# Kernel optimization log

Hardware: AMD Instinct MI355X
Metric: run time of the kernel (lower is better)

The kernel has to match this reference:

```python
import jax, jax.numpy as jnp
import numpy as np

TPB = 64          # tokens_per_block
SUB = 16          # sub_chunk_size
BUDGET = 1024     # dynamic_sparse_token_budget
ROPE_BASE = 10000.0
NEG = -1e9


def rope_neox(x, pos, base=ROPE_BASE):
    # neox-style rotary over full head_dim, single position `pos`
    D = x.shape[-1]
    half = D // 2
    inv_freq = 1.0 / (base ** (jnp.arange(half, dtype=jnp.float32) * (2.0 / D)))
    ang = pos * inv_freq
    c, s = jnp.cos(ang), jnp.sin(ang)
    x1, x2 = x[..., :half], x[..., half:]
    return jnp.concatenate([x1 * c - x2 * s, x1 * s + x2 * c], axis=-1)


def setup_inputs() -> dict:
    key = jax.random.key(0)
    ks = jax.random.split(key, 8)
    B, H, Hkv, D = 4, 32, 8, 128
    P, S = 128, 64  # pages, tokens per page (memory_max_len=8192)
    q = jax.random.normal(ks[0], (B, H, D), dtype=jnp.float32)
    k = jax.random.normal(ks[1], (B, Hkv, D), dtype=jnp.float32)
    v = jax.random.normal(ks[2], (B, Hkv, D), dtype=jnp.float32)
    k_cache = jax.random.randint(ks[3], (B, P, S, Hkv, D), 0, 127, dtype=jnp.int32)
    v_cache = jax.random.randint(ks[4], (B, P, S, Hkv, D), 0, 127, dtype=jnp.int32)
    # per-tensor dequant scales for K and V (realistic small magnitudes)
    kv_scale_quant_orig = jax.random.uniform(ks[5], (2,), dtype=jnp.float32) * 0.02 + 0.005
    lengths_per_sample = jax.random.randint(ks[6], (4,), 4096, 8192, dtype=jnp.int32)
    return {
        'q': q, 'k': k, 'v': v,
        'kv_scale_quant_orig': kv_scale_quant_orig,
        'k_cache': k_cache, 'v_cache': v_cache,
        'lengths_per_sample': lengths_per_sample,
        'timestep': 8192,
    }


def reference(q, k, v, kv_scale_quant_orig, k_cache, v_cache, lengths_per_sample, timestep):
    B, H, D = q.shape
    Hkv = k.shape[1]
    G = H // Hkv  # GQA group size
    P, S = k_cache.shape[1], k_cache.shape[2]
    sm_scale = 1.0 / np.sqrt(D)
    pos = float(timestep - 1)  # rope_scaling_factor = 1.0

    # rotary on current query and current key
    qh = rope_neox(q, pos).reshape(B, Hkv, G, D)
    k_cur = rope_neox(k, pos)

    # int8 per-tensor dequant of paged KV cache -> [B, Hkv, P, S, D]
    sk, sv = kv_scale_quant_orig[0], kv_scale_quant_orig[1]
    kc = k_cache.astype(jnp.float32).transpose(0, 3, 1, 2, 4) * sk
    vc = v_cache.astype(jnp.float32).transpose(0, 3, 1, 2, 4) * sv

    lengths = jnp.maximum(lengths_per_sample, 1)

    # ---- dynamic top-k page selection (selector pass over full cache) ----
    scores = jnp.einsum('bhgd,bhpsd->bhgps', qh, kc) * sm_scale  # [B,Hkv,G,P,S]
    posgrid = jnp.arange(P * S, dtype=jnp.int32).reshape(P, S)
    valid = posgrid[None, None, None] < lengths[:, None, None, None, None]
    scores = jnp.where(valid, scores, NEG)
    # sub-chunk max stats then per-page max (== max over all tokens in page)
    page_stats = scores.reshape(B, Hkv, G, P, S // SUB, SUB).max(axis=-1).max(axis=-1)  # [B,Hkv,G,P]
    kk = min(max(3, BUDGET // TPB), P) - 1
    _, top_idx = jax.lax.top_k(page_stats[..., :-1], kk)
    last = jnp.full(top_idx.shape[:-1] + (1,), P - 1, dtype=top_idx.dtype)
    sel = jnp.concatenate([top_idx, last], axis=-1)  # [B,Hkv,G,Kp], last page forced
    Kp = sel.shape[-1]

    # ---- sparse attention over the selected pages + current token ----
    idx = sel[..., None, None]  # [B,Hkv,G,Kp,1,1]
    k_sel = jnp.take_along_axis(kc[:, :, None], idx, axis=3)  # [B,Hkv,G,Kp,S,D]
    v_sel = jnp.take_along_axis(vc[:, :, None], idx, axis=3)

    sel_scores = jnp.einsum('bhgd,bhgksd->bhgks', qh, k_sel) * sm_scale
    sel_pos = sel[..., None] * TPB + jnp.arange(S, dtype=jnp.int32)
    smask = sel_pos < lengths[:, None, None, None, None]
    sel_scores = jnp.where(smask, sel_scores, NEG)

    cur_score = jnp.einsum('bhgd,bhd->bhg', qh, k_cur) * sm_scale
    all_scores = jnp.concatenate(
        [sel_scores.reshape(B, Hkv, G, Kp * S), cur_score[..., None]], axis=-1)
    p = jax.nn.softmax(all_scores, axis=-1)

    v_all = jnp.concatenate(
        [v_sel.reshape(B, Hkv, G, Kp * S, D),
         jnp.broadcast_to(v[:, :, None, None, :], (B, Hkv, G, 1, D))], axis=3)
    out = jnp.einsum('bhgt,bhgtd->bhgd', p, v_all).reshape(B, H, D)
    selected_page_idx = sel.reshape(B, H, Kp).astype(jnp.int32)
    return out, selected_page_idx
```

## Files before the change

### kernel.cpp

```cpp
#include <hip/hip_runtime.h>
#include <hip/hip_bf16.h>

#define NB 4
#define NH 32
#define NHKV 8
#define NG 4
#define ND 128
#define NP 128
#define NS 64
#define KK 15
#define KP 16
#define NEGF -1000000000.0f
#define SM_SCALE 0.088388347648318447f

#define WS_QH   0
#define WS_KR   16384
#define WS_CUR  20480
#define WS_SC   20992
#define WS_ST   (WS_SC + NB*NHKV*NG*NP*NS)
#define WS_SEL  (WS_ST + NB*NHKV*NG*NP)
#define WS_PW   (WS_SEL + NB*NHKV*NG*KP)

__global__ __launch_bounds__(256) void prep_kernel(const float* __restrict__ q,
                                                   const float* __restrict__ k,
                                                   const int* __restrict__ tstep,
                                                   float* __restrict__ ws) {
    float* QH = ws + WS_QH;
    float* KR = ws + WS_KR;
    float* CUR = ws + WS_CUR;
    const float pos = (float)(tstep[0] - 1);
    const int tid = threadIdx.x;
    for (int i = tid; i < NB * NH * 64; i += 256) {
        int j = i & 63, head = i >> 6;
        float invf = 1.0f / powf(10000.0f, (float)j * (1.0f / 64.0f));
        float sng, csn;
        sincosf(pos * invf, &sng, &csn);
        float x1 = q[head * ND + j], x2 = q[head * ND + 64 + j];
        QH[head * ND + j] = x1 * csn - x2 * sng;
        QH[head * ND + 64 + j] = x1 * sng + x2 * csn;
    }
    for (int i = tid; i < NB * NHKV * 64; i += 256) {
        int j = i & 63, head = i >> 6;
        float invf = 1.0f / powf(10000.0f, (float)j * (1.0f / 64.0f));
        float sng, csn;
        sincosf(pos * invf, &sng, &csn);
        float x1 = k[head * ND + j], x2 = k[head * ND + 64 + j];
        KR[head * ND + j] = x1 * csn - x2 * sng;
        KR[head * ND + 64 + j] = x1 * sng + x2 * csn;
    }
    __syncthreads();
    for (int h = tid; h < NB * NH; h += 256) {
        int b = h >> 5, hh = h & 31, hkv = hh >> 2;
        const float* qr = QH + h * ND;
        const float* kr = KR + (b * NHKV + hkv) * ND;
        float acc = 0.f;
#pragma unroll 8
        for (int d = 0; d < ND; ++d) acc += qr[d] * kr[d];
        CUR[h] = acc * SM_SCALE;
    }
}

__global__ __launch_bounds__(256) void score_kernel(const int* __restrict__ kc,
                                                    const float* __restrict__ kvs,
                                                    const int* __restrict__ lens,
                                                    float* __restrict__ ws) {
    __shared__ float klds[NS][132];
    __shared__ float qlds[NG][ND];
    const float* QH = ws + WS_QH;
    float* SC = ws + WS_SC;
    float* ST = ws + WS_ST;
    const int blk = blockIdx.x;
    const int p = blk & (NP - 1);
    const int bh = blk >> 7;
    const int hkv = bh & (NHKV - 1);
    const int b = bh >> 3;
    const int len = max(lens[b], 1);
    const int tid = threadIdx.x;
    const int g = tid >> 6, s = tid & 63;
    const int bhg = (b * NHKV + hkv) * NG + g;
    if (p * NS >= len) {
        SC[bhg * (NP * NS) + p * NS + s] = NEGF;
        if (s == 0) ST[bhg * NP + p] = NEGF;
        return;
    }
    for (int i = tid; i < NG * ND; i += 256)
        qlds[i >> 7][i & 127] = QH[(b * NH + hkv * NG + (i >> 7)) * ND + (i & 127)];
    const int4* src = (const int4*)(kc + ((b * NP + p) * NS * NHKV + hkv) * ND);
    for (int i = tid; i < NS * 32; i += 256) {
        int ss = i >> 5, j = i & 31;
        int4 w = src[ss * (NHKV * ND / 4) + j];
        float4 f;
        f.x = (float)w.x; f.y = (float)w.y; f.z = (float)w.z; f.w = (float)w.w;
        *(float4*)&klds[ss][j * 4] = f;
    }
    __syncthreads();
    const float4* qrow = (const float4*)qlds[g];
    const float4* krow = (const float4*)&klds[s][0];
    float acc = 0.f;
#pragma unroll
    for (int j = 0; j < 32; ++j) {
        float4 qa = qrow[j], ka = krow[j];
        acc += qa.x * ka.x + qa.y * ka.y + qa.z * ka.z + qa.w * ka.w;
    }
    float score = acc * kvs[0] * SM_SCALE;
    if (p * NS + s >= len) score = NEGF;
    SC[bhg * (NP * NS) + p * NS + s] = score;
    float m = score;
#pragma unroll
    for (int off = 32; off; off >>= 1) m = fmaxf(m, __shfl_xor(m, off));
    if (s == 0) ST[bhg * NP + p] = m;
}

__global__ __launch_bounds__(256) void select_kernel(const float* __restrict__ v,
                                                     const float* __restrict__ kvs,
                                                     float* __restrict__ ws,
                                                     float* __restrict__ out) {
    const int bhg = blockIdx.x;
    const int b = bhg >> 5;
    const int hkv = (bhg >> 2) & 7;
    const int tid = threadIdx.x;
    const float* SC = ws + WS_SC;
    const float* ST = ws + WS_ST;
    const float* CUR = ws + WS_CUR;
    int* SEL = (int*)(ws + WS_SEL);
    float* PW = ws + WS_PW;
    __shared__ float st[NP];
    __shared__ int sel[KP];
    __shared__ float redm[4], reds[4];
    if (tid < NP) st[tid] = (tid < NP - 1) ? ST[bhg * NP + tid] : NEGF;
    __syncthreads();
    if (tid < 64) {
        for (int r = 0; r < KK; ++r) {
            float v1 = st[tid];
            int i1 = tid;
            float v2 = st[tid + 64];
            int i2 = tid + 64;
            if (v2 > v1) { v1 = v2; i1 = i2; }
#pragma unroll
            for (int off = 32; off; off >>= 1) {
                float ov = __shfl_xor(v1, off);
                int oi = __shfl_xor(i1, off);
                if (ov > v1 || (ov == v1 && oi < i1)) { v1 = ov; i1 = oi; }
            }
            if (tid == 0) sel[r] = i1;
            st[i1] = NEGF;
        }
        if (tid == 0) sel[KK] = NP - 1;
    }
    __syncthreads();
    if (tid < KP) {
        out[NB * NH * ND + bhg * KP + tid] = (float)sel[tid];
        SEL[bhg * KP + tid] = sel[tid];
    }
    float vals[4];
    float lm = NEGF;
    const float* scb = SC + bhg * (NP * NS);
#pragma unroll
    for (int u = 0; u < 4; ++u) {
        int idx = tid * 4 + u;
        int j = idx >> 6, s2 = idx & 63;
        float sc = scb[sel[j] * NS + s2];
        vals[u] = sc;
        lm = fmaxf(lm, sc);
    }
#pragma unroll
    for (int off = 32; off; off >>= 1) lm = fmaxf(lm, __shfl_xor(lm, off));
    if ((tid & 63) == 0) redm[tid >> 6] = lm;
    __syncthreads();
    const float cur = CUR[bhg];
    float m = fmaxf(fmaxf(redm[0], redm[1]), fmaxf(redm[2], redm[3]));
    m = fmaxf(m, cur);
    float e[4];
    float ls = 0.f;
#pragma unroll
    for (int u = 0; u < 4; ++u) {
        e[u] = expf(vals[u] - m);
        ls += e[u];
    }
#pragma unroll
    for (int off = 32; off; off >>= 1) ls += __shfl_xor(ls, off);
    if ((tid & 63) == 0) reds[tid >> 6] = ls;
    __syncthreads();
    float ecur = expf(cur - m);
    float Z = reds[0] + reds[1] + reds[2] + reds[3] + ecur;
    float inv = 1.0f / Z;
    float pscale = inv * kvs[1];
#pragma unroll
    for (int u = 0; u < 4; ++u) PW[bhg * 1024 + tid * 4 + u] = e[u] * pscale;
    if (tid < ND)
        out[bhg * ND + tid] = (ecur * inv) * v[(b * NHKV + hkv) * ND + tid];
}

__global__ __launch_bounds__(128) void pv_kernel(const int* __restrict__ vc,
                                                 float* __restrict__ ws,
                                                 float* __restrict__ out) {
    const int blk = blockIdx.x;
    const int bhg = blk >> 4;
    const int j = blk & 15;
    const int b = bhg >> 5;
    const int hkv = (bhg >> 2) & 7;
    const int* SEL = (const int*)(ws + WS_SEL);
    const float* PW = ws + WS_PW;
    __shared__ float pl[NS];
    __shared__ float4 red[128];
    const int tid = threadIdx.x;
    if (tid < NS) pl[tid] = PW[bhg * 1024 + j * NS + tid];
    const int page = SEL[bhg * KP + j];
    __syncthreads();
    const int4* vb = (const int4*)(vc + ((b * NP + page) * NS * NHKV + hkv) * ND);
    const int j4 = tid & 31;
    const int s0 = tid >> 5;
    float4 acc = {0.f, 0.f, 0.f, 0.f};
#pragma unroll
    for (int s = s0; s < NS; s += 4) {
        int4 w = vb[s * (NHKV * ND / 4) + j4];
        float pv = pl[s];
        acc.x += pv * (float)w.x;
        acc.y += pv * (float)w.y;
        acc.z += pv * (float)w.z;
        acc.w += pv * (float)w.w;
    }
    red[tid] = acc;
    __syncthreads();
    if (tid < 32) {
        float4 a = red[tid], b2 = red[tid + 32], c = red[tid + 64], d2 = red[tid + 96];
        float x = a.x + b2.x + c.x + d2.x;
        float y = a.y + b2.y + c.y + d2.y;
        float z = a.z + b2.z + c.z + d2.z;
        float w = a.w + b2.w + c.w + d2.w;
        float* o = &out[bhg * ND + tid * 4];
        atomicAdd(o + 0, x);
        atomicAdd(o + 1, y);
        atomicAdd(o + 2, z);
        atomicAdd(o + 3, w);
    }
}

extern "C" void kernel_launch(void* const* d_in, const int* in_sizes, int n_in,
                              void* d_out, int out_size, void* d_ws, size_t ws_size,
                              hipStream_t stream) {
    const float* q = (const float*)d_in[0];
    const float* k = (const float*)d_in[1];
    const float* v = (const float*)d_in[2];
    const float* kvs = (const float*)d_in[3];
    const int* kc = (const int*)d_in[4];
    const int* vc = (const int*)d_in[5];
    const int* lens = (const int*)d_in[6];
    const int* tstep = (const int*)d_in[7];
    float* out = (float*)d_out;
    float* ws = (float*)d_ws;

    prep_kernel<<<1, 256, 0, stream>>>(q, k, tstep, ws);
    score_kernel<<<NB * NHKV * NP, 256, 0, stream>>>(kc, kvs, lens, ws);
    select_kernel<<<NB * NHKV * NG, 256, 0, stream>>>(v, kvs, ws, out);
    pv_kernel<<<NB * NHKV * NG * KP, 128, 0, stream>>>(vc, ws, out);
}
```

Before: 306.8 us.

## Fuse RoPE prep into score and select kernels, XOR-swizzle K tile in LDS

Removes the single-block prep kernel by recomputing rotary embedding of q inside each score block and of q/k plus the current-token score inside each select block. This drops a serial launch and a tiny one-block kernel from the critical path. Separately, the padded K tile in LDS is replaced by an XOR-swizzled layout to avoid bank conflicts without padding. The cost is redundant powf/sincos work per block.

Result: faster. 285.4 us (-7.0%).

```diff
diff --git a/kernel.cpp b/kernel.cpp
--- a/kernel.cpp
+++ b/kernel.cpp
@@ -1,5 +1,4 @@
 #include <hip/hip_runtime.h>
-#include <hip/hip_bf16.h>
 
 #define NB 4
 #define NH 32
@@ -13,60 +12,23 @@
 #define NEGF -1000000000.0f
 #define SM_SCALE 0.088388347648318447f
 
-#define WS_QH   0
-#define WS_KR   16384
-#define WS_CUR  20480
-#define WS_SC   20992
-#define WS_ST   (WS_SC + NB*NHKV*NG*NP*NS)
+#define WS_SC   0
+#define WS_ST   (NB*NHKV*NG*NP*NS)
 #define WS_SEL  (WS_ST + NB*NHKV*NG*NP)
 #define WS_PW   (WS_SEL + NB*NHKV*NG*KP)
 
-__global__ __launch_bounds__(256) void prep_kernel(const float* __restrict__ q,
-                                                   const float* __restrict__ k,
-                                                   const int* __restrict__ tstep,
-                                                   float* __restrict__ ws) {
-    float* QH = ws + WS_QH;
-    float* KR = ws + WS_KR;
-    float* CUR = ws + WS_CUR;
-    const float pos = (float)(tstep[0] - 1);
-    const int tid = threadIdx.x;
-    for (int i = tid; i < NB * NH * 64; i += 256) {
-        int j = i & 63, head = i >> 6;
-        float invf = 1.0f / powf(10000.0f, (float)j * (1.0f / 64.0f));
-        float sng, csn;
-        sincosf(pos * invf, &sng, &csn);
-        float x1 = q[head * ND + j], x2 = q[head * ND + 64 + j];
-        QH[head * ND + j] = x1 * csn - x2 * sng;
-        QH[head * ND + 64 + j] = x1 * sng + x2 * csn;
-    }
-    for (int i = tid; i < NB * NHKV * 64; i += 256) {
-        int j = i & 63, head = i >> 6;
-        float invf = 1.0f / powf(10000.0f, (float)j * (1.0f / 64.0f));
-        float sng, csn;
-        sincosf(pos * invf, &sng, &csn);
-        float x1 = k[head * ND + j], x2 = k[head * ND + 64 + j];
-        KR[head * ND + j] = x1 * csn - x2 * sng;
-        KR[head * ND + 64 + j] = x1 * sng + x2 * csn;
-    }
-    __syncthreads();
-    for (int h = tid; h < NB * NH; h += 256) {
-        int b = h >> 5, hh = h & 31, hkv = hh >> 2;
-        const float* qr = QH + h * ND;
-        const float* kr = KR + (b * NHKV + hkv) * ND;
-        float acc = 0.f;
-#pragma unroll 8
-        for (int d = 0; d < ND; ++d) acc += qr[d] * kr[d];
-        CUR[h] = acc * SM_SCALE;
-    }
-}
-
-__global__ __launch_bounds__(256) void score_kernel(const int* __restrict__ kc,
+__device__ __forceinline__ float ref_invfreq(int j) {
+    return 1.0f / powf(10000.0f, (float)j * (1.0f / 64.0f));
+}
+
+__global__ __launch_bounds__(256) void score_kernel(const float* __restrict__ q,
+                                                    const int* __restrict__ kc,
                                                     const float* __restrict__ kvs,
                                                     const int* __restrict__ lens,
+                                                    const int* __restrict__ tstep,
                                                     float* __restrict__ ws) {
-    __shared__ float klds[NS][132];
+    __shared__ float klds[NS][ND];
     __shared__ float qlds[NG][ND];
-    const float* QH = ws + WS_QH;
     float* SC = ws + WS_SC;
     float* ST = ws + WS_ST;
     const int blk = blockIdx.x;
@@ -83,23 +45,35 @@
         if (s == 0) ST[bhg * NP + p] = NEGF;
         return;
     }
-    for (int i = tid; i < NG * ND; i += 256)
-        qlds[i >> 7][i & 127] = QH[(b * NH + hkv * NG + (i >> 7)) * ND + (i & 127)];
+    {
+        const float pos = (float)(tstep[0] - 1);
+        const int j = s;
+        const float invf = ref_invfreq(j);
+        float sn, cs;
+        sincosf(pos * invf, &sn, &cs);
+        const float* qh = q + (b * NH + hkv * NG + g) * ND;
+        float x1 = qh[j], x2 = qh[64 + j];
+        qlds[g][j] = x1 * cs - x2 * sn;
+        qlds[g][64 + j] = x1 * sn + x2 * cs;
+    }
     const int4* src = (const int4*)(kc + ((b * NP + p) * NS * NHKV + hkv) * ND);
     for (int i = tid; i < NS * 32; i += 256) {
         int ss = i >> 5, j = i & 31;
         int4 w = src[ss * (NHKV * ND / 4) + j];
         float4 f;
         f.x = (float)w.x; f.y = (float)w.y; f.z = (float)w.z; f.w = (float)w.w;
-        *(float4*)&klds[ss][j * 4] = f;
+        int c = j ^ (ss & 31);
+        *(float4*)&klds[ss][c * 4] = f;
     }
     __syncthreads();
     const float4* qrow = (const float4*)qlds[g];
-    const float4* krow = (const float4*)&klds[s][0];
+    const float* kl0 = &klds[0][0];
+    const int cbase = s * ND + ((s & 31) << 2);
     float acc = 0.f;
 #pragma unroll
-    for (int j = 0; j < 32; ++j) {
-        float4 qa = qrow[j], ka = krow[j];
+    for (int jj = 0; jj < 32; ++jj) {
+        float4 qa = qrow[jj];
+        float4 ka = *(const float4*)&kl0[cbase ^ (jj << 2)];
         acc += qa.x * ka.x + qa.y * ka.y + qa.z * ka.z + qa.w * ka.w;
     }
     float score = acc * kvs[0] * SM_SCALE;
@@ -111,25 +85,53 @@
     if (s == 0) ST[bhg * NP + p] = m;
 }
 
-__global__ __launch_bounds__(256) void select_kernel(const float* __restrict__ v,
+__global__ __launch_bounds__(256) void select_kernel(const float* __restrict__ q,
+                                                     const float* __restrict__ k,
+                                                     const float* __restrict__ v,
                                                      const float* __restrict__ kvs,
+                                                     const int* __restrict__ tstep,
                                                      float* __restrict__ ws,
                                                      float* __restrict__ out) {
     const int bhg = blockIdx.x;
     const int b = bhg >> 5;
     const int hkv = (bhg >> 2) & 7;
+    const int g = bhg & 3;
     const int tid = threadIdx.x;
     const float* SC = ws + WS_SC;
     const float* ST = ws + WS_ST;
-    const float* CUR = ws + WS_CUR;
     int* SEL = (int*)(ws + WS_SEL);
     float* PW = ws + WS_PW;
+    __shared__ float qh2[ND], kr2[ND], pr[128];
     __shared__ float st[NP];
     __shared__ int sel[KP];
-    __shared__ float redm[4], reds[4];
+    __shared__ float redm[4], reds[4], curS;
+    const float pos = (float)(tstep[0] - 1);
+    if (tid < 128) {
+        int j = tid & 63;
+        const float invf = ref_invfreq(j);
+        float sn, cs;
+        sincosf(pos * invf, &sn, &cs);
+        if (tid < 64) {
+            const float* qh = q + (b * NH + hkv * NG + g) * ND;
+            float x1 = qh[j], x2 = qh[64 + j];
+            qh2[j] = x1 * cs - x2 * sn;
+            qh2[64 + j] = x1 * sn + x2 * cs;
+        } else {
+            const float* kh = k + (b * NHKV + hkv) * ND;
+            float x1 = kh[j], x2 = kh[64 + j];
+            kr2[j] = x1 * cs - x2 * sn;
+            kr2[64 + j] = x1 * sn + x2 * cs;
+        }
+    }
     if (tid < NP) st[tid] = (tid < NP - 1) ? ST[bhg * NP + tid] : NEGF;
     __syncthreads();
+    if (tid < 128) pr[tid] = qh2[tid] * kr2[tid];
+    __syncthreads();
     if (tid < 64) {
+        float val = pr[tid] + pr[tid + 64];
+#pragma unroll
+        for (int off = 32; off; off >>= 1) val += __shfl_xor(val, off);
+        if (tid == 0) curS = val * SM_SCALE;
         for (int r = 0; r < KK; ++r) {
             float v1 = st[tid];
             int i1 = tid;
@@ -167,7 +169,7 @@
     for (int off = 32; off; off >>= 1) lm = fmaxf(lm, __shfl_xor(lm, off));
     if ((tid & 63) == 0) redm[tid >> 6] = lm;
     __syncthreads();
-    const float cur = CUR[bhg];
+    const float cur = curS;
     float m = fmaxf(fmaxf(redm[0], redm[1]), fmaxf(redm[2], redm[3]));
     m = fmaxf(m, cur);
     float e[4];
@@ -250,8 +252,7 @@
     float* out = (float*)d_out;
     float* ws = (float*)d_ws;
 
-    prep_kernel<<<1, 256, 0, stream>>>(q, k, tstep, ws);
-    score_kernel<<<NB * NHKV * NP, 256, 0, stream>>>(kc, kvs, lens, ws);
-    select_kernel<<<NB * NHKV * NG, 256, 0, stream>>>(v, kvs, ws, out);
+    score_kernel<<<NB * NHKV * NP, 256, 0, stream>>>(q, kc, kvs, lens, tstep, ws);
+    select_kernel<<<NB * NHKV * NG, 256, 0, stream>>>(q, k, v, kvs, tstep, ws, out);
     pv_kernel<<<NB * NHKV * NG * KP, 128, 0, stream>>>(vc, ws, out);
 }
```
